# Performance work log

Hardware: AMD Instinct MI355X
Metric: run time of the kernel (lower is better)

## Reference

```python
import jax, jax.numpy as jnp
import numpy as np

N = 50000      # nodes
E = 800000     # edges (before self-loops)
D_IN = 64
D_OUT = 64


def setup_inputs() -> dict:
    key = jax.random.key(0)
    k1, k2, k3 = jax.random.split(key, 3)
    x = jax.random.normal(k1, (N, D_IN), dtype=jnp.float32)
    edge_index = jax.random.randint(k2, (2, E), 0, N, dtype=jnp.int64)
    # Glorot-ish init for the GCN linear weight
    W = jax.random.normal(k3, (D_IN, D_OUT), dtype=jnp.float32) * (1.0 / np.sqrt(D_IN))
    b = jnp.zeros((D_OUT,), dtype=jnp.float32)
    return {"x": x, "edge_index": edge_index, "W": W, "b": b}


def reference(x, edge_index, W, b):
    # GCNConv: add self-loops, symmetric normalization D^-1/2 (A+I) D^-1/2,
    # linear transform, scatter-add aggregation, bias; then ReLU.
    # Dropout is treated in eval mode (identity) for determinism.
    n = x.shape[0]
    loop = jnp.arange(n, dtype=edge_index.dtype)
    src = jnp.concatenate([edge_index[0], loop])  # [E+N]
    dst = jnp.concatenate([edge_index[1], loop])  # [E+N]

    ones = jnp.ones(src.shape[0], dtype=x.dtype)
    deg = jax.ops.segment_sum(ones, dst, num_segments=n)            # [N]
    dis = jnp.where(deg > 0, jax.lax.rsqrt(deg), 0.0)               # deg^-1/2
    norm = dis[src] * dis[dst]                                      # [E+N]

    xw = x @ W                                                      # [N, D_OUT]
    msgs = norm[:, None] * xw[src]                                  # [E+N, D_OUT]
    out = jax.ops.segment_sum(msgs, dst, num_segments=n) + b        # [N, D_OUT]
    return jax.nn.relu(out)
```

## Files before the change

kernel.cpp:

```cpp
#include <hip/hip_runtime.h>


#define TPB 256
#define STPB 512
#define MAXDEG 64
#define OVFCAP 8192
#define EPB 2048
#define MAXBIN 1024
#define MAXBLK 512
#define LUTSZ 2048

typedef float fvec4 __attribute__((ext_vector_type(4)));

__device__ __forceinline__ int edges_are_i32(const unsigned* __restrict__ w) {
    int lane = threadIdx.x & 63;
    unsigned v = w[1 + 2 * lane];
    return __ballot(v != 0u) != 0ull;
}

__device__ __forceinline__ unsigned short f2bf(float f) {
    unsigned u = __float_as_uint(f);
    u += 0x7FFFu + ((u >> 16) & 1u);
    return (unsigned short)(u >> 16);
}
__device__ __forceinline__ float bf2f(unsigned short h) {
    return __uint_as_float(((unsigned)h) << 16);
}
__device__ __forceinline__ unsigned scale2(unsigned v, float dd) {
    unsigned lo = (unsigned)f2bf(dd * bf2f((unsigned short)(v & 0xFFFFu)));
    unsigned hi = (unsigned)f2bf(dd * bf2f((unsigned short)(v >> 16)));
    return lo | (hi << 16);
}

__device__ __forceinline__ void load4(const void* ei, int is32, long long base, int* v) {
    if (is32) {
        int4 a = *(const int4*)((const int*)ei + base);
        v[0] = a.x; v[1] = a.y; v[2] = a.z; v[3] = a.w;
    } else {
        longlong4 a = *(const longlong4*)((const long long*)ei + base);
        v[0] = (int)a.x; v[1] = (int)a.y; v[2] = (int)a.z; v[3] = (int)a.w;
    }
}

__global__ __launch_bounds__(512) void gemm_binsort(
        const float* __restrict__ x, const float* __restrict__ W,
        unsigned short* __restrict__ z0, unsigned* __restrict__ ovf,
        const void* __restrict__ ei, unsigned* __restrict__ arena,
        uint2* __restrict__ desc, int E, int nbins, int nblocks,
        int n, int gemmBlocks) {
    __shared__ __align__(16) unsigned char smem[22528];
    const int t = threadIdx.x;

    if ((int)blockIdx.x < gemmBlocks) {
        if (blockIdx.x == 0 && t == 0) *ovf = 0u;
        float* lw = (float*)smem;
#pragma unroll
        for (int i = 0; i < 8; ++i) lw[i * 512 + t] = W[i * 512 + t];
        __syncthreads();

        const int lane = t & 63;
        const int wv   = t >> 6;
        const int row0 = blockIdx.x * 64 + wv * 8;
        if (row0 >= n) return;
        const int nr = (n - row0 >= 8) ? 8 : (n - row0);

        float acc[8] = {0.f, 0.f, 0.f, 0.f, 0.f, 0.f, 0.f, 0.f};
#pragma unroll
        for (int k0 = 0; k0 < 16; ++k0) {
            const float w0 = lw[(4 * k0 + 0) * 64 + lane];
            const float w1 = lw[(4 * k0 + 1) * 64 + lane];
            const float w2 = lw[(4 * k0 + 2) * 64 + lane];
            const float w3 = lw[(4 * k0 + 3) * 64 + lane];
#pragma unroll
            for (int r = 0; r < 8; ++r) {
                if (r < nr) {
                    float4 xv = *(const float4*)(x + (long long)(row0 + r) * 64 + 4 * k0);
                    acc[r] = fmaf(xv.w, w3, fmaf(xv.z, w2, fmaf(xv.y, w1,
                             fmaf(xv.x, w0, acc[r]))));
                }
            }
        }
#pragma unroll
        for (int r = 0; r < 8; ++r)
            if (r < nr) z0[(long long)(row0 + r) * 64 + lane] = f2bf(acc[r]);
        return;
    }

    unsigned* hist    = (unsigned*)smem;
    unsigned* bstart  = hist + MAXBIN;
    unsigned* cur     = bstart + MAXBIN;
    unsigned* sorted  = cur + MAXBIN;
    unsigned* partial = sorted + EPB;
    const int blk = (int)blockIdx.x - gemmBlocks;
    const long long base = (long long)blk * EPB;
    const int cnt = (int)((E - base < EPB) ? (E - base) : EPB);
    const int is32 = edges_are_i32((const unsigned*)ei);

    for (int i = t; i < nbins; i += STPB) hist[i] = 0u;
    __syncthreads();

    unsigned pay[4];
    unsigned short bn[4];
    {
        const int lo = t * 4;
        if (lo + 4 <= cnt) {
            int s4[4], d4[4];
            load4(ei, is32, base + lo, s4);
            load4(ei, is32, (long long)E + base + lo, d4);
#pragma unroll
            for (int k = 0; k < 4; ++k) {
                pay[k] = ((unsigned)(d4[k] & 63) << 16) | (unsigned)s4[k];
                bn[k]  = (unsigned short)((unsigned)d4[k] >> 6);
                atomicAdd(&hist[bn[k]], 1u);
            }
        } else {
#pragma unroll
            for (int k = 0; k < 4; ++k) {
                int l = lo + k;
                if (l < cnt) {
                    int s_, d_;
                    if (is32) {
                        s_ = ((const int*)ei)[base + l];
                        d_ = ((const int*)ei)[(long long)E + base + l];
                    } else {
                        s_ = (int)((const long long*)ei)[base + l];
                        d_ = (int)((const long long*)ei)[(long long)E + base + l];
                    }
                    pay[k] = ((unsigned)(d_ & 63) << 16) | (unsigned)s_;
                    bn[k]  = (unsigned short)((unsigned)d_ >> 6);
                    atomicAdd(&hist[bn[k]], 1u);
                } else {
                    bn[k] = 0xFFFFu;
                }
            }
        }
    }
    __syncthreads();

    unsigned s0 = 0;
#pragma unroll
    for (int k = 0; k < 2; ++k) { int bq = t * 2 + k; if (bq < nbins) s0 += hist[bq]; }
    partial[t] = s0;
    __syncthreads();
    for (int o = 1; o < STPB; o <<= 1) {
        unsigned v = (t >= o) ? partial[t - o] : 0u;
        __syncthreads();
        partial[t] += v;
        __syncthreads();
    }
    unsigned run = (t == 0) ? 0u : partial[t - 1];
#pragma unroll
    for (int k = 0; k < 2; ++k) {
        int bq = t * 2 + k;
        if (bq < nbins) { bstart[bq] = run; cur[bq] = run; run += hist[bq]; }
    }
    __syncthreads();

#pragma unroll
    for (int i = 0; i < 4; ++i) {
        if (bn[i] != 0xFFFFu) {
            unsigned p = atomicAdd(&cur[bn[i]], 1u);
            sorted[p] = pay[i];
        }
    }
    __syncthreads();

    for (int i = t; i < cnt; i += STPB) arena[base + i] = sorted[i];
    for (int bq = t; bq < nbins; bq += STPB) {
        uint2 dd;
        dd.x = (unsigned)(base + bstart[bq]);
        dd.y = hist[bq];
        desc[(long long)blk * nbins + bq] = dd;
    }
}

__global__ __launch_bounds__(256) void build_ell(const uint2* __restrict__ desc,
                                                 const unsigned* __restrict__ arena,
                                                 unsigned* __restrict__ fc,
                                                 unsigned short* __restrict__ ell,
                                                 unsigned* __restrict__ ovf,
                                                 int* __restrict__ ovfList,
                                                 unsigned short* __restrict__ z,
                                                 int n, int nbins, int nblocks) {
    __shared__ unsigned segstart[MAXBLK];
    __shared__ unsigned segpre[MAXBLK];
    __shared__ unsigned pre[MAXBLK];
    __shared__ unsigned lcnt[MAXDEG];
    __shared__ unsigned short lut[LUTSZ];
    __shared__ __align__(16) unsigned short lell[MAXDEG * MAXDEG];
    const int t   = threadIdx.x;
    const int bin = blockIdx.x;
    const int base = bin * MAXDEG;

    if (t < MAXDEG) lcnt[t] = 0u;

    unsigned len0 = 0, len1 = 0;
    if (t < nblocks) {
        uint2 dd = desc[(long long)t * nbins + bin];
        segstart[t] = dd.x;
        len0 = dd.y;
    }
    if (t + 256 < nblocks) {
        uint2 dd = desc[(long long)(t + 256) * nbins + bin];
        segstart[t + 256] = dd.x;
        len1 = dd.y;
    }
    pre[t] = len0;
    pre[t + 256] = len1;
    __syncthreads();
    for (int o = 1; o < 256; o <<= 1) {
        unsigned vA = (t >= o) ? pre[t - o] : 0u;
        unsigned vB = (t >= o) ? pre[256 + t - o] : 0u;
        __syncthreads();
        pre[t] += vA;
        pre[256 + t] += vB;
        __syncthreads();
    }
    const unsigned lowTot = pre[255];
    pre[256 + t] += lowTot;
    __syncthreads();
    const unsigned total = pre[MAXBLK - 1];
    unsigned sp0 = 0, sp1 = 0;
    if (t < nblocks) { sp0 = pre[t] - len0; segpre[t] = sp0; }
    if (t + 256 < nblocks) { sp1 = pre[256 + t] - len1; segpre[t + 256] = sp1; }
    __syncthreads();

    for (unsigned k = 0; k < len0 && sp0 + k < LUTSZ; ++k)
        lut[sp0 + k] = (unsigned short)t;
    for (unsigned k = 0; k < len1 && sp1 + k < LUTSZ; ++k)
        lut[sp1 + k] = (unsigned short)(t + 256);
    __syncthreads();

    for (unsigned j = t; j < total; j += 256) {
        int lo;
        if (j < LUTSZ) {
            lo = (int)lut[j];
        } else {
            int l = 0, hi = nblocks - 1;
            while (l < hi) {
                int mid = (l + hi + 1) >> 1;
                if (segpre[mid] <= j) l = mid; else hi = mid - 1;
            }
            lo = l;
        }
        unsigned e  = arena[segstart[lo] + (j - segpre[lo])];
        unsigned dl = e >> 16;
        unsigned c  = atomicAdd(&lcnt[dl], 1u);
        if (c < MAXDEG) {
            lell[dl * MAXDEG + c] = (unsigned short)(e & 0xFFFFu);
        } else {
            unsigned p = atomicAdd(ovf, 1u);
            if (p < OVFCAP) {
                ovfList[2 * p]     = (int)(e & 0xFFFFu);
                ovfList[2 * p + 1] = base + (int)dl;
            }
        }
    }
    __syncthreads();

    const int maxrow = (n - base < MAXDEG) ? (n - base) : MAXDEG;
    if (t < maxrow) fc[base + t] = lcnt[t];

    const uint4* lp = (const uint4*)lell;
    uint4* gp = (uint4*)(ell + (long long)base * MAXDEG);
    for (int i = t; i < maxrow * 8; i += 256) gp[i] = lp[i];

    uint4* zp = (uint4*)(z + (long long)base * 64);
    for (int i = t; i < maxrow * 8; i += 256) {
        int row = i >> 3;
        float dd = rsqrtf(1.0f + (float)lcnt[row]);
        uint4 v = zp[i];
        v.x = scale2(v.x, dd); v.y = scale2(v.y, dd);
        v.z = scale2(v.z, dd); v.w = scale2(v.w, dd);
        zp[i] = v;
    }
}

__global__ __launch_bounds__(256) void gather_z(const unsigned short* __restrict__ ell,
                                                const unsigned* __restrict__ fc,
                                                const unsigned* __restrict__ ovf,
                                                const int* __restrict__ ovfList,
                                                const unsigned short* __restrict__ z,
                                                const float* __restrict__ b,
                                                float* __restrict__ out, int n) {
    const int wv   = (int)threadIdx.x >> 6;
    const int lane = threadIdx.x & 63;
    const int o    = lane >> 3;
    const int cp   = lane & 7;
    const int node = (blockIdx.x * 4 + wv) * 8 + o;
    const bool valid = node < n;
    const int nodec = valid ? node : (n - 1);

    const unsigned deg = valid ? fc[nodec] : 0u;
    const float dd = rsqrtf(1.0f + (float)deg);

    uint4 zs = *(const uint4*)(z + (unsigned)nodec * 64 + cp * 8);
    float a0 = bf2f((unsigned short)(zs.x & 0xFFFFu));
    float a1 = bf2f((unsigned short)(zs.x >> 16));
    float a2 = bf2f((unsigned short)(zs.y & 0xFFFFu));
    float a3 = bf2f((unsigned short)(zs.y >> 16));
    float a4 = bf2f((unsigned short)(zs.z & 0xFFFFu));
    float a5 = bf2f((unsigned short)(zs.z >> 16));
    float a6 = bf2f((unsigned short)(zs.w & 0xFFFFu));
    float a7 = bf2f((unsigned short)(zs.w >> 16));

    unsigned m = deg < MAXDEG ? deg : MAXDEG;
    if (!valid) m = 0u;
    unsigned mm = m;
    {
        unsigned q1 = (unsigned)__shfl_xor((int)mm, 8);  mm = mm > q1 ? mm : q1;
        unsigned q2 = (unsigned)__shfl_xor((int)mm, 16); mm = mm > q2 ? mm : q2;
        unsigned q3 = (unsigned)__shfl_xor((int)mm, 32); mm = mm > q3 ? mm : q3;
    }
    const unsigned mmax = mm;

    const uint4* prow = (const uint4*)(ell + (unsigned)nodec * MAXDEG);

    unsigned i = 0;
    for (; i + 8 <= mmax; i += 8) {
        uint4 rw = prow[i >> 3];
        unsigned s[8];
        s[0] = rw.x & 0xFFFFu; s[1] = rw.x >> 16;
        s[2] = rw.y & 0xFFFFu; s[3] = rw.y >> 16;
        s[4] = rw.z & 0xFFFFu; s[5] = rw.z >> 16;
        s[6] = rw.w & 0xFFFFu; s[7] = rw.w >> 16;
        if (i + 8 <= m) {
            uint4 v[8];
#pragma unroll
            for (int k = 0; k < 8; ++k)
                v[k] = *(const uint4*)(z + s[k] * 64u + cp * 8);
#pragma unroll
            for (int k = 0; k < 8; ++k) {
                a0 += bf2f((unsigned short)(v[k].x & 0xFFFFu));
                a1 += bf2f((unsigned short)(v[k].x >> 16));
                a2 += bf2f((unsigned short)(v[k].y & 0xFFFFu));
                a3 += bf2f((unsigned short)(v[k].y >> 16));
                a4 += bf2f((unsigned short)(v[k].z & 0xFFFFu));
                a5 += bf2f((unsigned short)(v[k].z >> 16));
                a6 += bf2f((unsigned short)(v[k].w & 0xFFFFu));
                a7 += bf2f((unsigned short)(v[k].w >> 16));
            }
        } else {
#pragma unroll
            for (int k = 0; k < 8; ++k) {
                if (i + k < m) {
                    uint4 v = *(const uint4*)(z + s[k] * 64u + cp * 8);
                    a0 += bf2f((unsigned short)(v.x & 0xFFFFu));
                    a1 += bf2f((unsigned short)(v.x >> 16));
                    a2 += bf2f((unsigned short)(v.y & 0xFFFFu));
                    a3 += bf2f((unsigned short)(v.y >> 16));
                    a4 += bf2f((unsigned short)(v.z & 0xFFFFu));
                    a5 += bf2f((unsigned short)(v.z >> 16));
                    a6 += bf2f((unsigned short)(v.w & 0xFFFFu));
                    a7 += bf2f((unsigned short)(v.w >> 16));
                }
            }
        }
    }
    for (; i < mmax; ++i) {
        if (i < m) {
            unsigned s = ell[(unsigned)nodec * MAXDEG + i];
            uint4 v = *(const uint4*)(z + s * 64u + cp * 8);
            a0 += bf2f((unsigned short)(v.x & 0xFFFFu));
            a1 += bf2f((unsigned short)(v.x >> 16));
            a2 += bf2f((unsigned short)(v.y & 0xFFFFu));
            a3 += bf2f((unsigned short)(v.y >> 16));
            a4 += bf2f((unsigned short)(v.z & 0xFFFFu));
            a5 += bf2f((unsigned short)(v.z >> 16));
            a6 += bf2f((unsigned short)(v.w & 0xFFFFu));
            a7 += bf2f((unsigned short)(v.w >> 16));
        }
    }

    unsigned nov = *ovf;
    if (nov > 0) {
        nov = nov < OVFCAP ? nov : OVFCAP;
        for (unsigned j = 0; j < nov; ++j)
            if (valid && ovfList[2 * j + 1] == node) {
                uint4 v = *(const uint4*)(z + (unsigned)ovfList[2 * j] * 64u + cp * 8);
                a0 += bf2f((unsigned short)(v.x & 0xFFFFu));
                a1 += bf2f((unsigned short)(v.x >> 16));
                a2 += bf2f((unsigned short)(v.y & 0xFFFFu));
                a3 += bf2f((unsigned short)(v.y >> 16));
                a4 += bf2f((unsigned short)(v.z & 0xFFFFu));
                a5 += bf2f((unsigned short)(v.z >> 16));
                a6 += bf2f((unsigned short)(v.w & 0xFFFFu));
                a7 += bf2f((unsigned short)(v.w >> 16));
            }
    }

    if (valid) {
        float4 b0 = *(const float4*)(b + cp * 8);
        float4 b1 = *(const float4*)(b + cp * 8 + 4);
        fvec4 o0, o1;
        o0.x = fmaxf(fmaf(dd, a0, b0.x), 0.f);
        o0.y = fmaxf(fmaf(dd, a1, b0.y), 0.f);
        o0.z = fmaxf(fmaf(dd, a2, b0.z), 0.f);
        o0.w = fmaxf(fmaf(dd, a3, b0.w), 0.f);
        o1.x = fmaxf(fmaf(dd, a4, b1.x), 0.f);
        o1.y = fmaxf(fmaf(dd, a5, b1.y), 0.f);
        o1.z = fmaxf(fmaf(dd, a6, b1.z), 0.f);
        o1.w = fmaxf(fmaf(dd, a7, b1.w), 0.f);
        __builtin_nontemporal_store(o0, (fvec4*)(out + (unsigned)node * 64 + cp * 8));
        __builtin_nontemporal_store(o1, (fvec4*)(out + (unsigned)node * 64 + cp * 8 + 4));
    }
}

extern "C" void kernel_launch(void* const* d_in, const int* in_sizes, int n_in,
                              void* d_out, int out_size, void* d_ws, size_t ws_size,
                              hipStream_t stream) {
    const float* x  = (const float*)d_in[0];
    const void*  ei = d_in[1];
    const float* W  = (const float*)d_in[2];
    const float* b  = (const float*)d_in[3];
    float* out = (float*)d_out;

    const int n = in_sizes[0] / 64;
    const int E = in_sizes[1] / 2;
    const int nbins   = (n + MAXDEG - 1) / MAXDEG;
    const int nblocks = (E + EPB - 1) / EPB;
    const int gemmBlocks = (n + 63) / 64;

    unsigned short* z       = (unsigned short*)d_ws;
    unsigned short* ell     = z + (long long)n * 64;
    unsigned*       fc      = (unsigned*)(ell + (long long)n * 64);
    unsigned*       ovf     = fc + n;
    int*            ovfList = (int*)(ovf + 1);
    unsigned*       arena   = (unsigned*)(ovfList + 2 * OVFCAP);
    uint2*          desc    = (uint2*)(arena + E);

    gemm_binsort<<<gemmBlocks + nblocks, STPB, 0, stream>>>(
        x, W, z, ovf, ei, arena, desc, E, nbins, nblocks, n, gemmBlocks);
    build_ell<<<nbins, TPB, 0, stream>>>(desc, arena, fc, ell, ovf, ovfList, z,
                                         n, nbins, nblocks);
    gather_z<<<(n + 31) / 32, TPB, 0, stream>>>(ell, fc, ovf, ovfList, z, b, out, n);
}
```

Before: 76.06 us.

## Pack bin descriptors into one word, use wave-shuffle scan, widen gather blocks

The per-bin segment descriptor shrinks from uint2 to a single 32-bit word (start<<12 | len). This halves desc write and read traffic between the binsort and ELL-build kernels. The block-wide LDS Hillis-Steele scan, which needed many barriers, becomes a wave-level shuffle scan plus an 8-entry wave-sum pass, and the bstart array is dropped to cut shared memory. gather_z moves to 512-thread blocks. Packing limits start offsets to 20 bits (about 1M edges) and segment lengths to 12 bits, which fits E=800k but is fragile for larger inputs.

```diff
diff --git a/kernel.cpp b/kernel.cpp
--- a/kernel.cpp
+++ b/kernel.cpp
@@ -46,9 +46,9 @@
         const float* __restrict__ x, const float* __restrict__ W,
         unsigned short* __restrict__ z0, unsigned* __restrict__ ovf,
         const void* __restrict__ ei, unsigned* __restrict__ arena,
-        uint2* __restrict__ desc, int E, int nbins, int nblocks,
+        unsigned* __restrict__ desc, int E, int nbins, int nblocks,
         int n, int gemmBlocks) {
-    __shared__ __align__(16) unsigned char smem[22528];
+    __shared__ __align__(16) unsigned char smem[16416];
     const int t = threadIdx.x;
 
     if ((int)blockIdx.x < gemmBlocks) {
@@ -86,15 +86,16 @@
         return;
     }
 
-    unsigned* hist    = (unsigned*)smem;
-    unsigned* bstart  = hist + MAXBIN;
-    unsigned* cur     = bstart + MAXBIN;
-    unsigned* sorted  = cur + MAXBIN;
-    unsigned* partial = sorted + EPB;
+    unsigned* hist   = (unsigned*)smem;
+    unsigned* cur    = hist + MAXBIN;
+    unsigned* sorted = cur + MAXBIN;
+    unsigned* wsum   = sorted + EPB;
     const int blk = (int)blockIdx.x - gemmBlocks;
     const long long base = (long long)blk * EPB;
     const int cnt = (int)((E - base < EPB) ? (E - base) : EPB);
     const int is32 = edges_are_i32((const unsigned*)ei);
+    const int lane = t & 63;
+    const int wid  = t >> 6;
 
     for (int i = t; i < nbins; i += STPB) hist[i] = 0u;
     __syncthreads();
@@ -137,23 +138,24 @@
     }
     __syncthreads();
 
-    unsigned s0 = 0;
-#pragma unroll
-    for (int k = 0; k < 2; ++k) { int bq = t * 2 + k; if (bq < nbins) s0 += hist[bq]; }
-    partial[t] = s0;
-    __syncthreads();
-    for (int o = 1; o < STPB; o <<= 1) {
-        unsigned v = (t >= o) ? partial[t - o] : 0u;
-        __syncthreads();
-        partial[t] += v;
-        __syncthreads();
-    }
-    unsigned run = (t == 0) ? 0u : partial[t - 1];
-#pragma unroll
-    for (int k = 0; k < 2; ++k) {
-        int bq = t * 2 + k;
-        if (bq < nbins) { bstart[bq] = run; cur[bq] = run; run += hist[bq]; }
-    }
+    const int bq0 = t * 2, bq1 = t * 2 + 1;
+    unsigned h0 = (bq0 < nbins) ? hist[bq0] : 0u;
+    unsigned h1 = (bq1 < nbins) ? hist[bq1] : 0u;
+    unsigned s0 = h0 + h1;
+    unsigned xsc = s0;
+#pragma unroll
+    for (int o = 1; o < 64; o <<= 1) {
+        unsigned v = (unsigned)__shfl_up((int)xsc, o);
+        if (lane >= o) xsc += v;
+    }
+    if (lane == 63) wsum[wid] = xsc;
+    __syncthreads();
+    unsigned woff = 0;
+#pragma unroll
+    for (int w = 0; w < 8; ++w) woff += (w < wid) ? wsum[w] : 0u;
+    const unsigned excl = xsc + woff - s0;
+    if (bq0 < nbins) cur[bq0] = excl;
+    if (bq1 < nbins) cur[bq1] = excl + h0;
     __syncthreads();
 
 #pragma unroll
@@ -167,14 +169,14 @@
 
     for (int i = t; i < cnt; i += STPB) arena[base + i] = sorted[i];
     for (int bq = t; bq < nbins; bq += STPB) {
-        uint2 dd;
-        dd.x = (unsigned)(base + bstart[bq]);
-        dd.y = hist[bq];
-        desc[(long long)blk * nbins + bq] = dd;
-    }
-}
-
-__global__ __launch_bounds__(256) void build_ell(const uint2* __restrict__ desc,
+        unsigned len   = hist[bq];
+        unsigned start = cur[bq] - len;
+        desc[(long long)blk * nbins + bq] =
+            (((unsigned)base + start) << 12) | len;
+    }
+}
+
+__global__ __launch_bounds__(256) void build_ell(const unsigned* __restrict__ desc,
                                                  const unsigned* __restrict__ arena,
                                                  unsigned* __restrict__ fc,
                                                  unsigned short* __restrict__ ell,
@@ -196,14 +198,14 @@
 
     unsigned len0 = 0, len1 = 0;
     if (t < nblocks) {
-        uint2 dd = desc[(long long)t * nbins + bin];
-        segstart[t] = dd.x;
-        len0 = dd.y;
+        unsigned dd = desc[(long long)t * nbins + bin];
+        segstart[t] = dd >> 12;
+        len0 = dd & 0xFFFu;
     }
     if (t + 256 < nblocks) {
-        uint2 dd = desc[(long long)(t + 256) * nbins + bin];
-        segstart[t + 256] = dd.x;
-        len1 = dd.y;
+        unsigned dd = desc[(long long)(t + 256) * nbins + bin];
+        segstart[t + 256] = dd >> 12;
+        len1 = dd & 0xFFFu;
     }
     pre[t] = len0;
     pre[t + 256] = len1;
@@ -276,7 +278,7 @@
     }
 }
 
-__global__ __launch_bounds__(256) void gather_z(const unsigned short* __restrict__ ell,
+__global__ __launch_bounds__(512) void gather_z(const unsigned short* __restrict__ ell,
                                                 const unsigned* __restrict__ fc,
                                                 const unsigned* __restrict__ ovf,
                                                 const int* __restrict__ ovfList,
@@ -287,7 +289,7 @@
     const int lane = threadIdx.x & 63;
     const int o    = lane >> 3;
     const int cp   = lane & 7;
-    const int node = (blockIdx.x * 4 + wv) * 8 + o;
+    const int node = (blockIdx.x * 8 + wv) * 8 + o;
     const bool valid = node < n;
     const int nodec = valid ? node : (n - 1);
 
@@ -427,11 +429,11 @@
     unsigned*       ovf     = fc + n;
     int*            ovfList = (int*)(ovf + 1);
     unsigned*       arena   = (unsigned*)(ovfList + 2 * OVFCAP);
-    uint2*          desc    = (uint2*)(arena + E);
+    unsigned*       desc    = arena + E;
 
     gemm_binsort<<<gemmBlocks + nblocks, STPB, 0, stream>>>(
         x, W, z, ovf, ei, arena, desc, E, nbins, nblocks, n, gemmBlocks);
     build_ell<<<nbins, TPB, 0, stream>>>(desc, arena, fc, ell, ovf, ovfList, z,
                                          n, nbins, nblocks);
-    gather_z<<<(n + 31) / 32, TPB, 0, stream>>>(ell, fc, ovf, ovfList, z, b, out, n);
-}
+    gather_z<<<(n + 63) / 64, STPB, 0, stream>>>(ell, fc, ovf, ovfList, z, b, out, n);
+}
```

Result: no change. 76.58 us (+0.7%).
